# Optimization experiments

Measured on AMD Instinct MI355X. Metric: run time of the kernel, lower is better.

Reference implementation:

```python
import jax, jax.numpy as jnp
import numpy as np

N_NODES = 100000
N_EDGES = 400000
N_GRAPHS = 4096
BN_EPS = 1e-5


def _glorot(key, shape):
    fan_in, fan_out = shape
    lim = np.sqrt(6.0 / (fan_in + fan_out))
    return jax.random.uniform(key, shape, jnp.float32, -lim, lim)


def setup_inputs() -> dict:
    key = jax.random.key(0)
    ks = jax.random.split(key, 16)
    x = jax.random.normal(ks[0], (N_NODES, 373), jnp.float32)
    edge_index = jax.random.randint(ks[1], (2, N_EDGES), 0, N_NODES, jnp.int64)
    batch = jnp.sort(jax.random.randint(ks[2], (N_NODES,), 0, N_GRAPHS, jnp.int64))
    params = {
        # GIN layer 1 MLP: 373->256->256
        'W1a': _glorot(ks[3], (373, 256)), 'b1a': jnp.zeros((256,), jnp.float32),
        'W1b': _glorot(ks[4], (256, 256)), 'b1b': jnp.zeros((256,), jnp.float32),
        'g1': jnp.ones((256,), jnp.float32), 'be1': jnp.zeros((256,), jnp.float32),
        # GIN layer 2 MLP: 256->128->128
        'W2a': _glorot(ks[5], (256, 128)), 'b2a': jnp.zeros((128,), jnp.float32),
        'W2b': _glorot(ks[6], (128, 128)), 'b2b': jnp.zeros((128,), jnp.float32),
        'g2': jnp.ones((128,), jnp.float32), 'be2': jnp.zeros((128,), jnp.float32),
        # GIN layer 3 MLP: 128->64->64
        'W3a': _glorot(ks[7], (128, 64)), 'b3a': jnp.zeros((64,), jnp.float32),
        'W3b': _glorot(ks[8], (64, 64)), 'b3b': jnp.zeros((64,), jnp.float32),
        'g3': jnp.ones((64,), jnp.float32), 'be3': jnp.zeros((64,), jnp.float32),
        # head
        'Wf1': _glorot(ks[9], (64, 16)), 'bf1': jnp.zeros((16,), jnp.float32),
        'Wf2': _glorot(ks[10], (16, 1)), 'bf2': jnp.zeros((1,), jnp.float32),
    }
    return {'x': x, 'edge_index': edge_index, 'batch': batch, **params}


def _gin_conv(x, src, dst, Wa, ba, Wb, bb):
    # sum-aggregate neighbor messages (eps = 0 default in GINConv)
    agg = jax.ops.segment_sum(x[src], dst, num_segments=N_NODES)
    h = x + agg
    h = jax.nn.relu(h @ Wa + ba) @ Wb + bb
    return h


def _batchnorm(x, gamma, beta):
    mu = jnp.mean(x, axis=0)
    var = jnp.var(x, axis=0)
    return (x - mu) * jax.lax.rsqrt(var + BN_EPS) * gamma + beta


def reference(x, edge_index, batch,
              W1a, b1a, W1b, b1b, g1, be1,
              W2a, b2a, W2b, b2b, g2, be2,
              W3a, b3a, W3b, b3b, g3, be3,
              Wf1, bf1, Wf2, bf2):
    src, dst = edge_index[0], edge_index[1]
    h = jax.nn.relu(_gin_conv(x, src, dst, W1a, b1a, W1b, b1b))
    h = _batchnorm(h, g1, be1)
    h = jax.nn.relu(_gin_conv(h, src, dst, W2a, b2a, W2b, b2b))
    h = _batchnorm(h, g2, be2)
    h = jax.nn.relu(_gin_conv(h, src, dst, W3a, b3a, W3b, b3b))
    h = _batchnorm(h, g3, be3)
    # global_add_pool: [N, 64] -> [G, 64]
    pooled = jax.ops.segment_sum(h, batch, num_segments=N_GRAPHS)
    out = jax.nn.relu(pooled @ Wf1 + bf1)
    # dropout omitted (eval mode)
    out = jax.nn.relu(out @ Wf2 + bf2)
    return out.reshape(-1)
```

## Files before the change

kernel.cpp:

```cpp
#include <hip/hip_runtime.h>

#define N_NODES 100000
#define N_EDGES 400000
#define N_GRAPHS 4096
#define BN_EPS 1e-5f
#define DEG_CAP 32

typedef unsigned short ushort_t;
typedef short short8 __attribute__((ext_vector_type(8)));
typedef unsigned short ushort4v __attribute__((ext_vector_type(4)));
typedef unsigned short ushort8v __attribute__((ext_vector_type(8)));
typedef float floatx4 __attribute__((ext_vector_type(4)));

__device__ __forceinline__ ushort_t f2b(float f) {
    union { float f; unsigned u; } v; v.f = f;
    unsigned r = v.u + 0x7fffu + ((v.u >> 16) & 1u);
    return (ushort_t)(r >> 16);
}
__device__ __forceinline__ float b2f(ushort_t b) {
    union { unsigned u; float f; } v; v.u = ((unsigned)b) << 16;
    return v.f;
}

__global__ void k_pad_x(const float* __restrict__ x, ushort_t* __restrict__ xb,
                        int* __restrict__ cursor,
                        const float* __restrict__ W1a, ushort_t* __restrict__ BT1) {
    int t = threadIdx.x;
    if (blockIdx.x >= N_NODES) {
        int b = blockIdx.x - N_NODES;
        int n = b / 3, kc = b % 3;
        int k = kc * 128 + t;
        float v = (k < 373) ? W1a[(long)k * 256 + n] : 0.f;
        BT1[(long)n * 384 + k] = f2b(v);
        return;
    }
    int n = blockIdx.x;
    const float* xr = x + (long)n * 373;
    ushort_t* o = xb + (long)n * 384;
    if (t < 93) {
        float v0 = xr[t * 4 + 0], v1 = xr[t * 4 + 1], v2 = xr[t * 4 + 2], v3 = xr[t * 4 + 3];
        ushort4v s = {f2b(v0), f2b(v1), f2b(v2), f2b(v3)};
        *(ushort4v*)(o + t * 4) = s;
    } else if (t == 93) {
        o[372] = f2b(xr[372]);
        o[373] = 0; o[374] = 0; o[375] = 0;
    } else if (t == 94 || t == 95) {
        ushort4v z = {0, 0, 0, 0};
        *(ushort4v*)(o + 376 + (t - 94) * 4) = z;
    } else if (t == 96) {
        cursor[n] = 0;
    }
}

__global__ void k_fill(const int* __restrict__ src, const int* __restrict__ dst,
                       int* __restrict__ cursor, int* __restrict__ elist) {
    int e = blockIdx.x * blockDim.x + threadIdx.x;
    if (e < N_EDGES) {
        int d = dst[e];
        int slot = atomicAdd(&cursor[d], 1);
        if (slot < DEG_CAP) elist[(long)d * DEG_CAP + slot] = src[e];
    }
}

__global__ void k_prep_scaled(const float* __restrict__ W, const float* __restrict__ scsh,
                              ushort_t* __restrict__ BT, float* __restrict__ biasE,
                              int K, int Kp, int Nn) {
    int n = blockIdx.y;
    int k = blockIdx.x * 128 + threadIdx.x;
    if (k < Kp) {
        float v = (k < K) ? W[(long)k * Nn + n] * scsh[k] : 0.f;
        BT[(long)n * Kp + k] = f2b(v);
    }
    if (blockIdx.x == 0) {
        __shared__ float red[2];
        float s = 0.f;
        for (int kk = threadIdx.x; kk < K; kk += 128) s += scsh[K + kk] * W[(long)kk * Nn + n];
#pragma unroll
        for (int off = 32; off >= 1; off >>= 1) s += __shfl_xor(s, off);
        if ((threadIdx.x & 63) == 0) red[threadIdx.x >> 6] = s;
        __syncthreads();
        if (threadIdx.x == 0) biasE[n] = red[0] + red[1];
    }
}

template<int KP, int TN, bool STATS>
__global__ __launch_bounds__(256) void k_gemm(const ushort_t* __restrict__ A,
                                              const ushort_t* __restrict__ BT,
                                              const float* __restrict__ bias,
                                              ushort_t* __restrict__ C,
                                              float* __restrict__ partials,
                                              int M, int Nn, int relu) {
    __shared__ __align__(16) ushort_t As[2][128 * 32];
    __shared__ __align__(16) ushort_t Bs[2][TN * 32];
    float* swred = (float*)As;
    const int tid = threadIdx.x;
    const int wave = tid >> 6, lane = tid & 63;
    const int ln = lane & 15, kg = lane >> 4;
    const long rowBase = (long)blockIdx.y * 128;
    const int colBase = blockIdx.x * TN;

    constexpr int RT = (TN == 128) ? 4 : 2;
    const int rowOff = (TN == 128) ? ((wave >> 1) * 64) : (wave * 32);
    const int colOff = (TN == 128) ? ((wave & 1) * 64) : 0;

    const ushort_t* aSrc[2];
#pragma unroll
    for (int i = 0; i < 2; i++) {
        long r = rowBase + i * 64 + (tid >> 2);
        if (r >= M) r = M - 1;
        aSrc[i] = A + r * KP + (tid & 3) * 8;
    }
    const ushort_t* bSrc[TN / 64];
#pragma unroll
    for (int i = 0; i < TN / 64; i++) {
        long cc = colBase + i * 64 + (tid >> 2);
        bSrc[i] = BT + cc * KP + (tid & 3) * 8;
    }

    auto stage = [&](int b, int k0) {
#pragma unroll
        for (int i = 0; i < 2; i++)
            __builtin_amdgcn_global_load_lds(
                (const __attribute__((address_space(1))) void*)(aSrc[i] + k0),
                (__attribute__((address_space(3))) void*)(As[b] + wave * 512 + i * 2048), 16, 0, 0);
#pragma unroll
        for (int i = 0; i < TN / 64; i++)
            __builtin_amdgcn_global_load_lds(
                (const __attribute__((address_space(1))) void*)(bSrc[i] + k0),
                (__attribute__((address_space(3))) void*)(Bs[b] + wave * 512 + i * 2048), 16, 0, 0);
    };

    floatx4 acc[RT][4];
#pragma unroll
    for (int i = 0; i < RT; i++)
#pragma unroll
        for (int j = 0; j < 4; j++) acc[i][j] = (floatx4){0.f, 0.f, 0.f, 0.f};

    stage(0, 0);
    int cur = 0;
    for (int k0 = 0; k0 < KP; k0 += 32) {
        __syncthreads();
        if (k0 + 32 < KP) stage(cur ^ 1, k0 + 32);

        short8 afr[RT], bfr[4];
#pragma unroll
        for (int rt = 0; rt < RT; rt++)
            afr[rt] = *(const short8*)&As[cur][(rowOff + rt * 16 + ln) * 32 + kg * 8];
#pragma unroll
        for (int tn = 0; tn < 4; tn++)
            bfr[tn] = *(const short8*)&Bs[cur][(colOff + tn * 16 + ln) * 32 + kg * 8];
#pragma unroll
        for (int rt = 0; rt < RT; rt++)
#pragma unroll
            for (int tn = 0; tn < 4; tn++)
                acc[rt][tn] = __builtin_amdgcn_mfma_f32_16x16x32_bf16(afr[rt], bfr[tn], acc[rt][tn], 0, 0, 0);
        cur ^= 1;
    }

    if constexpr (STATS) {
        __syncthreads();
        for (int i = tid; i < 4 * 2 * TN; i += 256) swred[i] = 0.f;
        __syncthreads();
    }

    float sums[4] = {0.f, 0.f, 0.f, 0.f};
    float sqs[4]  = {0.f, 0.f, 0.f, 0.f};
#pragma unroll
    for (int rt = 0; rt < RT; rt++) {
#pragma unroll
        for (int tn = 0; tn < 4; tn++) {
            int gc = colBase + colOff + tn * 16 + ln;
            float bv = bias ? bias[gc] : 0.f;
#pragma unroll
            for (int r = 0; r < 4; r++) {
                long gr = rowBase + rowOff + rt * 16 + kg * 4 + r;
                if (gr < M) {
                    float v = acc[rt][tn][r] + bv;
                    if (relu) v = fmaxf(v, 0.f);
                    ushort_t sb = f2b(v);
                    C[gr * Nn + gc] = sb;
                    if (STATS) {
                        float vb = b2f(sb);
                        sums[tn] += vb;
                        sqs[tn] += vb * vb;
                    }
                }
            }
        }
    }
    if constexpr (STATS) {
#pragma unroll
        for (int tn = 0; tn < 4; tn++) {
            float s = sums[tn], q = sqs[tn];
            s += __shfl_xor(s, 16); q += __shfl_xor(q, 16);
            s += __shfl_xor(s, 32); q += __shfl_xor(q, 32);
            if (kg == 0) {
                int c = colOff + tn * 16 + ln;
                swred[wave * 2 * TN + c] = s;
                swred[wave * 2 * TN + TN + c] = q;
            }
        }
        __syncthreads();
        const int by = blockIdx.y;
        const int gyd = gridDim.y;
        for (int c = tid; c < TN; c += 256) {
            float ssum = 0.f, ssq = 0.f;
#pragma unroll
            for (int w = 0; w < 4; w++) {
                ssum += swred[w * 2 * TN + c];
                ssq  += swred[w * 2 * TN + TN + c];
            }
            long gc = colBase + c;
            partials[gc * gyd + by] = ssum;
            partials[((long)Nn + gc) * gyd + by] = ssq;
        }
    }
}

template<int KP, int TN>
__global__ __launch_bounds__(256, 4) void k_gemm_agg(const ushort_t* __restrict__ y,
                                                  const int* __restrict__ cursor,
                                                  const int* __restrict__ elist,
                                                  const float* __restrict__ badd,
                                                  const ushort_t* __restrict__ BT,
                                                  const float* __restrict__ bias,
                                                  ushort_t* __restrict__ C,
                                                  float* __restrict__ partials,
                                                  int M, int Nn) {
    __shared__ __align__(16) ushort_t Af[128 * KP];
    __shared__ __align__(16) ushort_t Bs[TN * 32];
    float* swred = (float*)Af;
    const int tid = threadIdx.x;
    const int wave = tid >> 6, lane = tid & 63;
    const int ln = lane & 15, kg = lane >> 4;
    const long rowBase = (long)blockIdx.y * 128;
    constexpr int CPR = KP / 8;
    constexpr int TPR = CPR;
    constexpr int RPS = 256 / TPR;

    {
        const int lr = tid / TPR;
        const int ck = tid % TPR;
        const int c0 = ck * 8;
        float bd[8];
#pragma unroll
        for (int j = 0; j < 8; j++) bd[j] = badd[c0 + j];
        for (int s = 0; s < 128; s += RPS) {
            int r = s + lr;
            long gr = rowBase + r; if (gr >= M) gr = M - 1;
            int cnt = cursor[gr]; if (cnt > DEG_CAP) cnt = DEG_CAP;
            const int* el = elist + gr * DEG_CAP;
            int4 e0 = *(const int4*)el;
            int4 e1 = *(const int4*)(el + 4);
            int ids[8] = {e0.x, e0.y, e0.z, e0.w, e1.x, e1.y, e1.z, e1.w};
            ushort8v sv = *(const ushort8v*)(y + gr * KP + c0);
            ushort8v rr[8];
#pragma unroll
            for (int i = 0; i < 8; i++)
                if (i < cnt) rr[i] = *(const ushort8v*)(y + (long)ids[i] * KP + c0);
            float av[8];
#pragma unroll
            for (int j = 0; j < 8; j++) av[j] = b2f(sv[j]);
#pragma unroll
            for (int i = 0; i < 8; i++)
                if (i < cnt) {
#pragma unroll
                    for (int j = 0; j < 8; j++) av[j] += b2f(rr[i][j]);
                }
            for (int i = 8; i < cnt; i++) {
                ushort8v u = *(const ushort8v*)(y + (long)el[i] * KP + c0);
#pragma unroll
                for (int j = 0; j < 8; j++) av[j] += b2f(u[j]);
            }
            ushort8v ov;
#pragma unroll
            for (int j = 0; j < 8; j++) ov[j] = f2b(fmaxf(av[j] + bd[j], 0.f));
            int cks = ck ^ (r & (CPR - 1));
            *(ushort8v*)&Af[r * KP + cks * 8] = ov;
        }
    }

    constexpr int RT = (TN == 128) ? 4 : 2;
    const int rowOff = (TN == 128) ? ((wave >> 1) * 64) : (wave * 32);
    const int colOff = (TN == 128) ? ((wave & 1) * 64) : 0;
    const ushort_t* bSrc[TN / 64];
#pragma unroll
    for (int i = 0; i < TN / 64; i++) {
        long cc = i * 64 + (tid >> 2);
        bSrc[i] = BT + cc * KP + (tid & 3) * 8;
    }
    ushort_t* bDst = Bs + wave * 512;

    floatx4 acc[RT][4];
#pragma unroll
    for (int i = 0; i < RT; i++)
#pragma unroll
        for (int j = 0; j < 4; j++) acc[i][j] = (floatx4){0.f, 0.f, 0.f, 0.f};

    for (int k0 = 0; k0 < KP; k0 += 32) {
        __syncthreads();
#pragma unroll
        for (int i = 0; i < TN / 64; i++)
            __builtin_amdgcn_global_load_lds(
                (const __attribute__((address_space(1))) void*)(bSrc[i] + k0),
                (__attribute__((address_space(3))) void*)(bDst + i * 2048), 16, 0, 0);
        __syncthreads();

        short8 afr[RT], bfr[4];
#pragma unroll
        for (int rt = 0; rt < RT; rt++) {
            int row = rowOff + rt * 16 + ln;
            int cks = ((k0 >> 3) + kg) ^ (row & (CPR - 1));
            afr[rt] = *(const short8*)&Af[row * KP + cks * 8];
        }
#pragma unroll
        for (int tn = 0; tn < 4; tn++)
            bfr[tn] = *(const short8*)&Bs[(colOff + tn * 16 + ln) * 32 + kg * 8];
#pragma unroll
        for (int rt = 0; rt < RT; rt++)
#pragma unroll
            for (int tn = 0; tn < 4; tn++)
                acc[rt][tn] = __builtin_amdgcn_mfma_f32_16x16x32_bf16(afr[rt], bfr[tn], acc[rt][tn], 0, 0, 0);
    }

    __syncthreads();
    for (int i = tid; i < 4 * 2 * TN; i += 256) swred[i] = 0.f;
    __syncthreads();

    float sums[4] = {0.f, 0.f, 0.f, 0.f};
    float sqs[4]  = {0.f, 0.f, 0.f, 0.f};
#pragma unroll
    for (int rt = 0; rt < RT; rt++) {
#pragma unroll
        for (int tn = 0; tn < 4; tn++) {
            int gc = colOff + tn * 16 + ln;
            float bv = bias[gc];
#pragma unroll
            for (int r = 0; r < 4; r++) {
                long gr = rowBase + rowOff + rt * 16 + kg * 4 + r;
                if (gr < M) {
                    float v = fmaxf(acc[rt][tn][r] + bv, 0.f);
                    ushort_t sb = f2b(v);
                    C[gr * Nn + gc] = sb;
                    float vb = b2f(sb);
                    sums[tn] += vb;
                    sqs[tn] += vb * vb;
                }
            }
        }
    }
#pragma unroll
    for (int tn = 0; tn < 4; tn++) {
        float s = sums[tn], q = sqs[tn];
        s += __shfl_xor(s, 16); q += __shfl_xor(q, 16);
        s += __shfl_xor(s, 32); q += __shfl_xor(q, 32);
        if (kg == 0) {
            int c = colOff + tn * 16 + ln;
            swred[wave * 2 * TN + c] = s;
            swred[wave * 2 * TN + TN + c] = q;
        }
    }
    __syncthreads();
    const int by = blockIdx.y;
    const int gyd = gridDim.y;
    for (int c = tid; c < TN; c += 256) {
        float ssum = 0.f, ssq = 0.f;
#pragma unroll
        for (int w = 0; w < 4; w++) {
            ssum += swred[w * 2 * TN + c];
            ssq  += swred[w * 2 * TN + TN + c];
        }
        partials[(long)c * gyd + by] = ssum;
        partials[((long)Nn + c) * gyd + by] = ssq;
    }
}

template<int D>
__global__ void k_aggregate(const ushort_t* __restrict__ y, const int* __restrict__ cursor,
                            const int* __restrict__ elist, const float* __restrict__ badd,
                            ushort_t* __restrict__ out, int nblk,
                            const float* __restrict__ Wn, ushort_t* __restrict__ BTn,
                            int KWn, int NWn) {
    int t = threadIdx.x;
    if ((int)blockIdx.x >= nblk) {
        int b = blockIdx.x - nblk;
        BTn[(long)b * KWn + t] = f2b(Wn[(long)t * NWn + b]);
        return;
    }
    const int CG = D / 8;
    const int NPB = 256 / CG;
    int n = blockIdx.x * NPB + t / CG;
    int c = (t % CG) * 8;
    if (n >= N_NODES) return;
    int cnt = cursor[n];
    if (cnt > DEG_CAP) cnt = DEG_CAP;
    const int* el = elist + (long)n * DEG_CAP;
    int4 e0 = *(const int4*)el;
    int4 e1 = *(const int4*)(el + 4);
    int ids[8] = {e0.x, e0.y, e0.z, e0.w, e1.x, e1.y, e1.z, e1.w};
    ushort8v sv = *(const ushort8v*)(y + (long)n * D + c);
    ushort8v rr[8];
#pragma unroll
    for (int i = 0; i < 8; i++)
        if (i < cnt) rr[i] = *(const ushort8v*)(y + (long)ids[i] * D + c);
    float av[8];
#pragma unroll
    for (int j = 0; j < 8; j++) av[j] = b2f(sv[j]);
#pragma unroll
    for (int i = 0; i < 8; i++)
        if (i < cnt) {
#pragma unroll
            for (int j = 0; j < 8; j++) av[j] += b2f(rr[i][j]);
        }
    for (int i = 8; i < cnt; i++) {
        ushort8v u = *(const ushort8v*)(y + (long)el[i] * D + c);
#pragma unroll
        for (int j = 0; j < 8; j++) av[j] += b2f(u[j]);
    }
    ushort8v o;
#pragma unroll
    for (int j = 0; j < 8; j++) o[j] = f2b(fmaxf(av[j] + badd[c + j], 0.f));
    *(ushort8v*)(out + (long)n * D + c) = o;
}

__global__ void k_bn(const float* __restrict__ partials, int gy,
                     const float* __restrict__ gamma, const float* __restrict__ beta,
                     float* __restrict__ scsh, int K,
                     const float* __restrict__ Wn, ushort_t* __restrict__ BTn,
                     int KWn, int NWn) {
    int b = blockIdx.x;
    int t = threadIdx.x;
    if (b >= K) {
        int p = b - K;
        int nk = KWn >> 6;
        int n = p / nk, kc = p - n * nk;
        int k = kc * 64 + t;
        BTn[(long)n * KWn + k] = f2b(Wn[(long)k * NWn + n]);
        return;
    }
    const float* ps = partials + (long)b * gy;
    const float* pq = partials + (long)(K + b) * gy;
    float s = 0.f, q = 0.f;
    for (int i = t; i < gy; i += 64) { s += ps[i]; q += pq[i]; }
#pragma unroll
    for (int off = 32; off >= 1; off >>= 1) { s += __shfl_xor(s, off); q += __shfl_xor(q, off); }
    if (t == 0) {
        float invN = 1.0f / (float)N_NODES;
        float mu = s * invN;
        float var = fmaxf(q * invN - mu * mu, 0.f);
        float sc = rsqrtf(var + BN_EPS) * gamma[b];
        scsh[b] = sc;
        scsh[K + b] = beta[b] - mu * sc;
    }
}

__global__ void k_poolhead(const ushort_t* __restrict__ h, const int* __restrict__ batch,
                           const float* __restrict__ scsh,
                           const float* __restrict__ Wf1, const float* __restrict__ bf1,
                           const float* __restrict__ Wf2, const float* __restrict__ bf2,
                           float* __restrict__ out) {
    __shared__ float pl[64];
    __shared__ float hid[16];
    int g = blockIdx.x;
    int c = threadIdx.x;
    int lo = 0, hi = N_NODES;
    while (lo < hi) { int mid = (lo + hi) >> 1; if (batch[mid] < g) lo = mid + 1; else hi = mid; }
    int start = lo;
    hi = N_NODES;
    while (lo < hi) { int mid = (lo + hi) >> 1; if (batch[mid] < g + 1) lo = mid + 1; else hi = mid; }
    int end = lo;
    float s = 0.f;
    for (int r = start; r < end; r++) s += b2f(h[(long)r * 64 + c]);
    pl[c] = s * scsh[c] + scsh[64 + c] * (float)(end - start);
    __syncthreads();
    if (c < 16) {
        float sh = bf1[c];
        for (int j = 0; j < 64; j++) sh += pl[j] * Wf1[j * 16 + c];
        hid[c] = fmaxf(sh, 0.f);
    }
    __syncthreads();
    if (c == 0) {
        float o = bf2[0];
#pragma unroll
        for (int k = 0; k < 16; k++) o += hid[k] * Wf2[k];
        out[g] = fmaxf(o, 0.f);
    }
}

extern "C" void kernel_launch(void* const* d_in, const int* in_sizes, int n_in,
                              void* d_out, int out_size, void* d_ws, size_t ws_size,
                              hipStream_t stream) {
    const float* x    = (const float*)d_in[0];
    const int*  ei    = (const int*)d_in[1];
    const int*  batch = (const int*)d_in[2];
    const float* W1a = (const float*)d_in[3];
    const float* b1a = (const float*)d_in[4];
    const float* W1b = (const float*)d_in[5];
    const float* b1b = (const float*)d_in[6];
    const float* g1  = (const float*)d_in[7];
    const float* be1 = (const float*)d_in[8];
    const float* W2a = (const float*)d_in[9];
    const float* b2a = (const float*)d_in[10];
    const float* W2b = (const float*)d_in[11];
    const float* b2b = (const float*)d_in[12];
    const float* g2  = (const float*)d_in[13];
    const float* be2 = (const float*)d_in[14];
    const float* W3a = (const float*)d_in[15];
    const float* b3a = (const float*)d_in[16];
    const float* W3b = (const float*)d_in[17];
    const float* b3b = (const float*)d_in[18];
    const float* g3  = (const float*)d_in[19];
    const float* be3 = (const float*)d_in[20];
    const float* Wf1 = (const float*)d_in[21];
    const float* bf1 = (const float*)d_in[22];
    const float* Wf2 = (const float*)d_in[23];
    const float* bf2 = (const float*)d_in[24];

    const int N = N_NODES, E = N_EDGES;
    const int* src = ei;
    const int* dst = ei + E;
    const int gy = (N + 127) / 128;

    char* wp = (char*)d_ws;
    auto carve = [&](size_t bytes) {
        char* p = wp;
        wp += (bytes + 255) & ~(size_t)255;
        return (void*)p;
    };
    ushort_t* xb     = (ushort_t*)carve((size_t)N * 384 * 2);
    ushort_t* bufA   = (ushort_t*)carve((size_t)N * 256 * 2);
    ushort_t* bufB   = (ushort_t*)carve((size_t)N * 256 * 2);
    int*      elist  = (int*)carve((size_t)N * DEG_CAP * 4);
    int*      cursor = (int*)carve((size_t)N * 4);
    ushort_t* BT1    = (ushort_t*)carve((size_t)256 * 384 * 2);
    ushort_t* BT2    = (ushort_t*)carve((size_t)256 * 384 * 2);
    float*    scsh   = (float*)carve(512 * 4);
    float*    biasE  = (float*)carve(256 * 4);
    float*    partials = (float*)carve((size_t)2 * 256 * gy * 4);

    dim3 blk(256);

    k_pad_x<<<N + 768, 128, 0, stream>>>(x, xb, cursor, W1a, BT1);
    k_fill<<<(E + 255) / 256, blk, 0, stream>>>(src, dst, cursor, elist);

    k_gemm<384, 128, false><<<dim3(2, gy), blk, 0, stream>>>(xb, BT1, nullptr, bufA, nullptr, N, 256, 0);
    k_aggregate<256><<<12500 + 256, blk, 0, stream>>>(bufA, cursor, elist, b1a, bufB, 12500, W1b, BT2, 256, 256);
    k_gemm<256, 128, true><<<dim3(2, gy), blk, 0, stream>>>(bufB, BT2, b1b, bufA, partials, N, 256, 1);
    k_bn<<<256 + 256, 64, 0, stream>>>(partials, gy, g1, be1, scsh, 256, W2b, BT2, 128, 128);

    k_prep_scaled<<<dim3(2, 128), 128, 0, stream>>>(W2a, scsh, BT1, biasE, 256, 256, 128);
    k_gemm<256, 128, false><<<dim3(1, gy), blk, 0, stream>>>(bufA, BT1, biasE, bufB, nullptr, N, 128, 0);
    k_gemm_agg<128, 128><<<dim3(1, gy), blk, 0, stream>>>(bufB, cursor, elist, b2a, BT2, b2b, bufA, partials, N, 128);
    k_bn<<<128 + 64, 64, 0, stream>>>(partials, gy, g2, be2, scsh, 128, W3b, BT2, 64, 64);

    k_prep_scaled<<<dim3(1, 64), 128, 0, stream>>>(W3a, scsh, BT1, biasE, 128, 128, 64);
    k_gemm<128, 64, false><<<dim3(1, gy), blk, 0, stream>>>(bufA, BT1, biasE, bufB, nullptr, N, 64, 0);
    k_gemm_agg<64, 64><<<dim3(1, gy), blk, 0, stream>>>(bufB, cursor, elist, b3a, BT2, b3b, bufA, partials, N, 64);
    k_bn<<<64, 64, 0, stream>>>(partials, gy, g3, be3, scsh, 64, nullptr, nullptr, 64, 64);

    k_poolhead<<<N_GRAPHS, 64, 0, stream>>>(bufA, batch, scsh, Wf1, bf1, Wf2, bf2, (float*)d_out);
}
```

Measured before the change: 621.5 us.

## Fuse fp32-to-bf16 conversion of x into first GEMM via direct LDS loads

Removes the separate padding/conversion pass that wrote a bf16 copy of x, and instead has a new GEMM kernel load fp32 x rows directly into LDS with swizzled global_load_lds, converting to bf16 in registers before MFMA. The prep kernel now only zeroes the cursor and transposes W1a. This avoids writing and re-reading a 77MB intermediate, at the cost of twice the LDS footprint for A tiles, 4-byte unaligned loads from the 373-stride rows, and per-element conversion inside the inner loop. Padding columns beyond 373 are read from neighbouring rows but multiplied by zero weights; the last row's overread is redirected.

```diff
diff --git a/kernel.cpp b/kernel.cpp
--- a/kernel.cpp
+++ b/kernel.cpp
@@ -22,34 +22,20 @@
     return v.f;
 }
 
-__global__ void k_pad_x(const float* __restrict__ x, ushort_t* __restrict__ xb,
-                        int* __restrict__ cursor,
+__global__ void k_prep0(int* __restrict__ cursor,
                         const float* __restrict__ W1a, ushort_t* __restrict__ BT1) {
     int t = threadIdx.x;
-    if (blockIdx.x >= N_NODES) {
-        int b = blockIdx.x - N_NODES;
-        int n = b / 3, kc = b % 3;
-        int k = kc * 128 + t;
-        float v = (k < 373) ? W1a[(long)k * 256 + n] : 0.f;
-        BT1[(long)n * 384 + k] = f2b(v);
+    int b = blockIdx.x;
+    if (b < 782) {
+        int i = b * 128 + t;
+        if (i < N_NODES) cursor[i] = 0;
         return;
     }
-    int n = blockIdx.x;
-    const float* xr = x + (long)n * 373;
-    ushort_t* o = xb + (long)n * 384;
-    if (t < 93) {
-        float v0 = xr[t * 4 + 0], v1 = xr[t * 4 + 1], v2 = xr[t * 4 + 2], v3 = xr[t * 4 + 3];
-        ushort4v s = {f2b(v0), f2b(v1), f2b(v2), f2b(v3)};
-        *(ushort4v*)(o + t * 4) = s;
-    } else if (t == 93) {
-        o[372] = f2b(xr[372]);
-        o[373] = 0; o[374] = 0; o[375] = 0;
-    } else if (t == 94 || t == 95) {
-        ushort4v z = {0, 0, 0, 0};
-        *(ushort4v*)(o + 376 + (t - 94) * 4) = z;
-    } else if (t == 96) {
-        cursor[n] = 0;
-    }
+    b -= 782;
+    int n = b / 3, kc = b % 3;
+    int k = kc * 128 + t;
+    float v = (k < 373) ? W1a[(long)k * 256 + n] : 0.f;
+    BT1[(long)n * 384 + k] = f2b(v);
 }
 
 __global__ void k_fill(const int* __restrict__ src, const int* __restrict__ dst,
@@ -80,6 +66,97 @@
         if ((threadIdx.x & 63) == 0) red[threadIdx.x >> 6] = s;
         __syncthreads();
         if (threadIdx.x == 0) biasE[n] = red[0] + red[1];
+    }
+}
+
+__global__ __launch_bounds__(256) void k_gemm_x(const float* __restrict__ x,
+                                                const ushort_t* __restrict__ BT,
+                                                ushort_t* __restrict__ C, int M) {
+    __shared__ __align__(16) float    Af[2][128 * 32];
+    __shared__ __align__(16) ushort_t Bs[2][128 * 32];
+    const int tid = threadIdx.x;
+    const int wave = tid >> 6, lane = tid & 63;
+    const int ln = lane & 15, kg = lane >> 4;
+    const long rowBase = (long)blockIdx.y * 128;
+    const int colBase = blockIdx.x * 128;
+    const int rowOff = (wave >> 1) * 64;
+    const int colOff = (wave & 1) * 64;
+
+    const ushort_t* bSrc[2];
+#pragma unroll
+    for (int i = 0; i < 2; i++) {
+        long cc = colBase + i * 64 + (tid >> 2);
+        bSrc[i] = BT + cc * 384 + (tid & 3) * 8;
+    }
+
+    auto stage = [&](int b, int k0) {
+#pragma unroll
+        for (int j = 0; j < 16; j++) {
+            int id = j * 256 + tid;
+            int rr = id >> 5;
+            long r = rowBase + rr; if (r >= M) r = M - 1;
+            int lc = id & 31;
+            int gcol = (((lc >> 2) ^ (rr & 7)) << 2) + (lc & 3);
+            const float* p = x + r * 373 + k0 + gcol;
+            if (k0 == 352 && r == M - 1 && gcol >= 21) p = x + r * 373;
+            __builtin_amdgcn_global_load_lds(
+                (const __attribute__((address_space(1))) void*)p,
+                (__attribute__((address_space(3))) void*)((char*)Af[b] + j * 1024 + wave * 256), 4, 0, 0);
+        }
+#pragma unroll
+        for (int i = 0; i < 2; i++)
+            __builtin_amdgcn_global_load_lds(
+                (const __attribute__((address_space(1))) void*)(bSrc[i] + k0),
+                (__attribute__((address_space(3))) void*)((char*)Bs[b] + wave * 1024 + i * 4096), 16, 0, 0);
+    };
+
+    floatx4 acc[4][4];
+#pragma unroll
+    for (int i = 0; i < 4; i++)
+#pragma unroll
+        for (int j = 0; j < 4; j++) acc[i][j] = (floatx4){0.f, 0.f, 0.f, 0.f};
+
+    stage(0, 0);
+    int cur = 0;
+    for (int k0 = 0; k0 < 384; k0 += 32) {
+        __syncthreads();
+        if (k0 + 32 < 384) stage(cur ^ 1, k0 + 32);
+
+        short8 afr[4], bfr[4];
+#pragma unroll
+        for (int rt = 0; rt < 4; rt++) {
+            int row = rowOff + rt * 16 + ln;
+            int s0 = (2 * kg) ^ (row & 7);
+            int s1 = (2 * kg + 1) ^ (row & 7);
+            floatx4 a0 = *(const floatx4*)&Af[cur][row * 32 + s0 * 4];
+            floatx4 a1 = *(const floatx4*)&Af[cur][row * 32 + s1 * 4];
+            union { ushort_t h[8]; short8 s; } cv;
+            cv.h[0] = f2b(a0[0]); cv.h[1] = f2b(a0[1]); cv.h[2] = f2b(a0[2]); cv.h[3] = f2b(a0[3]);
+            cv.h[4] = f2b(a1[0]); cv.h[5] = f2b(a1[1]); cv.h[6] = f2b(a1[2]); cv.h[7] = f2b(a1[3]);
+            afr[rt] = cv.s;
+        }
+#pragma unroll
+        for (int tn = 0; tn < 4; tn++)
+            bfr[tn] = *(const short8*)&Bs[cur][(colOff + tn * 16 + ln) * 32 + kg * 8];
+#pragma unroll
+        for (int rt = 0; rt < 4; rt++)
+#pragma unroll
+            for (int tn = 0; tn < 4; tn++)
+                acc[rt][tn] = __builtin_amdgcn_mfma_f32_16x16x32_bf16(afr[rt], bfr[tn], acc[rt][tn], 0, 0, 0);
+        cur ^= 1;
+    }
+
+#pragma unroll
+    for (int rt = 0; rt < 4; rt++) {
+#pragma unroll
+        for (int tn = 0; tn < 4; tn++) {
+            int gc = colBase + colOff + tn * 16 + ln;
+#pragma unroll
+            for (int r = 0; r < 4; r++) {
+                long gr = rowBase + rowOff + rt * 16 + kg * 4 + r;
+                if (gr < M) C[gr * 256 + gc] = f2b(acc[rt][tn][r]);
+            }
+        }
     }
 }
 
@@ -527,7 +604,6 @@
         wp += (bytes + 255) & ~(size_t)255;
         return (void*)p;
     };
-    ushort_t* xb     = (ushort_t*)carve((size_t)N * 384 * 2);
     ushort_t* bufA   = (ushort_t*)carve((size_t)N * 256 * 2);
     ushort_t* bufB   = (ushort_t*)carve((size_t)N * 256 * 2);
     int*      elist  = (int*)carve((size_t)N * DEG_CAP * 4);
@@ -540,10 +616,10 @@
 
     dim3 blk(256);
 
-    k_pad_x<<<N + 768, 128, 0, stream>>>(x, xb, cursor, W1a, BT1);
+    k_prep0<<<782 + 768, 128, 0, stream>>>(cursor, W1a, BT1);
     k_fill<<<(E + 255) / 256, blk, 0, stream>>>(src, dst, cursor, elist);
 
-    k_gemm<384, 128, false><<<dim3(2, gy), blk, 0, stream>>>(xb, BT1, nullptr, bufA, nullptr, N, 256, 0);
+    k_gemm_x<<<dim3(2, gy), blk, 0, stream>>>(x, BT1, bufA, N);
     k_aggregate<256><<<12500 + 256, blk, 0, stream>>>(bufA, cursor, elist, b1a, bufB, 12500, W1b, BT2, 256, 256);
     k_gemm<256, 128, true><<<dim3(2, gy), blk, 0, stream>>>(bufB, BT2, b1b, bufA, partials, N, 256, 1);
     k_bn<<<256 + 256, 64, 0, stream>>>(partials, gy, g1, be1, scsh, 256, W2b, BT2, 128, 128);
```

New measurement: 617.9 us. Within noise of the previous version (-0.6%).
